# Performance work log

Hardware: AMD Instinct MI355X
Metric: run time of the kernel (lower is better)

Reference implementation:

```python
import jax, jax.numpy as jnp
import numpy as np

B, S, D = 4, 2048, 512

def setup_inputs() -> dict:
    key = jax.random.key(0)
    ks = jax.random.split(key, 7)
    # scale weights so unscaled logits stay in a sane softmax range
    w_scale = 0.05
    return {
        "x": jax.random.normal(ks[0], (B, S, D), dtype=jnp.float32),
        "W_q": jax.random.normal(ks[1], (D, D), dtype=jnp.float32) * w_scale,
        "W_k": jax.random.normal(ks[2], (D, D), dtype=jnp.float32) * w_scale,
        "W_v": jax.random.normal(ks[3], (D, D), dtype=jnp.float32) * w_scale,
        "b_q": jax.random.normal(ks[4], (D,), dtype=jnp.float32) * w_scale,
        "b_k": jax.random.normal(ks[5], (D,), dtype=jnp.float32) * w_scale,
        "b_v": jax.random.normal(ks[6], (D,), dtype=jnp.float32) * w_scale,
    }

def reference(x, W_q, W_k, W_v, b_q, b_k, b_v):
    # QKV projections: [B,S,D] @ [D,D] + [D]
    q = jnp.einsum('bsd,de->bse', x, W_q) + b_q
    k = jnp.einsum('bsd,de->bse', x, W_k) + b_k
    v = jnp.einsum('bsd,de->bse', x, W_v) + b_v
    # unscaled attention scores [B,S,S]
    scores = jnp.einsum('bqd,bkd->bqk', q, k)
    attn = jax.nn.softmax(scores, axis=-1)
    # weighted sum of values [B,S,D]
    return jnp.einsum('bqk,bkd->bqd', attn, v)
```

## Files before the change

### kernel.cpp

```cpp
#include <hip/hip_runtime.h>
#include <hip/hip_bf16.h>
#include <hip/hip_fp16.h>

#define BB 4
#define SS 2048
#define DD 512

typedef short s16x8 __attribute__((ext_vector_type(8)));
typedef short s16x4 __attribute__((ext_vector_type(4)));
typedef float f32x4 __attribute__((ext_vector_type(4)));
typedef _Float16 f16x8 __attribute__((ext_vector_type(8)));

__device__ __forceinline__ short f2h(float f) {
    const _Float16 h = (_Float16)f;
    union { _Float16 h; short s; } u; u.h = h; return u.s;
}
__device__ __forceinline__ float h2f(short s) {
    union { short s; _Float16 h; } u; u.s = s; return (float)u.h;
}
__device__ __forceinline__ f16x8 as_h(s16x8 v) {
    union { s16x8 s; f16x8 h; } u; u.s = v; return u.h;
}

__device__ __forceinline__ void gload_lds16(const void* g, void* l) {
    __builtin_amdgcn_global_load_lds(
        (const __attribute__((address_space(1))) void*)g,
        (__attribute__((address_space(3))) void*)l, 16, 0, 0);
}

__global__ __launch_bounds__(512, 2) void qkt256(
    const short* __restrict__ qf, const short* __restrict__ kf,
    short* __restrict__ outS, int nwg)
{
    __shared__ short lds[65536];

    const int tid = threadIdx.x;
    const int wave = tid >> 6, lane = tid & 63;
    const int flat = blockIdx.x + 8 * blockIdx.y + 64 * blockIdx.z;
    const int w = (flat & 7) * (nwg >> 3) + (flat >> 3);
    const int bm = ((w >> 3) & 7) * 256, bn = (w & 7) * 256;
    const long z = w >> 6;
    qf += z * (long)SS * DD; kf += z * (long)SS * DD;
    outS += z * (long)SS * SS;

    const int wm = (wave >> 2) * 128, wn = (wave & 3) * 64;
    const int lrow = lane & 15, lk16 = (lane >> 4) * 16;

    f32x4 acc[8][4] = {};

    auto base = [&](int buf, int arr) -> short* { return &lds[(buf * 2 + arr) * 8192]; };
    auto issue = [&](int buf, int arr, int k0) {
#pragma unroll
        for (int h = 0; h < 2; h++) {
            const int Lb = (h << 13) + (wave << 10) + (lane << 4);
            const int Ls = Lb ^ (((Lb >> 7) & 3) << 4);
            const int row = Ls >> 6, elem = (Ls & 63) >> 1;
            const short* s = arr ? kf : qf;
            const int rb = arr ? bn : bm;
            gload_lds16(s + (size_t)(rb + row) * DD + k0 + elem,
                        (char*)base(buf, arr) + Lb);
        }
    };
    auto rd = [&](int buf, int arr, int row) -> s16x8 {
        const int L = (row << 6) + lk16;
        const int Ls = L ^ (((L >> 7) & 3) << 4);
        return *(const s16x8*)((const char*)base(buf, arr) + Ls);
    };

#define QK_TILE(T, CUR, Bc, Bn, PREF)                                            \
  {                                                                              \
                                            \
    s16x8 aA0 = rd(CUR, 0, wm + 0 * 16 + lrow);                                  \
    s16x8 aA1 = rd(CUR, 0, wm + 1 * 16 + lrow);                                  \
    s16x8 aA2 = rd(CUR, 0, wm + 2 * 16 + lrow);                                  \
    s16x8 aA3 = rd(CUR, 0, wm + 3 * 16 + lrow);                                  \
    if (PREF) {                                                                  \
      issue((CUR) ^ 1, 1, ((T) + 1) * 32);                          \
      __builtin_amdgcn_sched_barrier(0);                                         \
      issue((CUR) ^ 1, 0, ((T) + 1) * 32);                         \
    }                                                                            \
    __builtin_amdgcn_s_barrier();                                                \
    asm volatile("s_waitcnt lgkmcnt(0)" ::: "memory");                           \
    __builtin_amdgcn_sched_barrier(0);                                           \
    __builtin_amdgcn_s_setprio(1);                                               \
    {                                                                            \
      _Pragma("unroll")                                                          \
      for (int n = 0; n < 4; n++) {                                              \
        acc[0][n] = __builtin_amdgcn_mfma_f32_16x16x32_f16(as_h(aA0), as_h(Bc[n]), acc[0][n], 0, 0, 0); \
        acc[1][n] = __builtin_amdgcn_mfma_f32_16x16x32_f16(as_h(aA1), as_h(Bc[n]), acc[1][n], 0, 0, 0); \
        acc[2][n] = __builtin_amdgcn_mfma_f32_16x16x32_f16(as_h(aA2), as_h(Bc[n]), acc[2][n], 0, 0, 0); \
        acc[3][n] = __builtin_amdgcn_mfma_f32_16x16x32_f16(as_h(aA3), as_h(Bc[n]), acc[3][n], 0, 0, 0); \
      }                                                                          \
    }                                                                            \
    __builtin_amdgcn_s_setprio(0);                                               \
    if (PREF) { asm volatile("s_waitcnt vmcnt(2)" ::: "memory");                 \
                __builtin_amdgcn_sched_barrier(0); }                             \
    __builtin_amdgcn_s_barrier();                                                \
                                            \
    aA0 = rd(CUR, 0, wm + 4 * 16 + lrow);                                        \
    aA1 = rd(CUR, 0, wm + 5 * 16 + lrow);                                        \
    aA2 = rd(CUR, 0, wm + 6 * 16 + lrow);                                        \
    aA3 = rd(CUR, 0, wm + 7 * 16 + lrow);                                        \
    if (PREF) {                                                                  \
      __builtin_amdgcn_sched_barrier(0);    \
      _Pragma("unroll")                                                          \
      for (int n = 0; n < 4; n++) {                                              \
        Bn[n] = rd((CUR) ^ 1, 1, wn + n * 16 + lrow);                            \
      }                                                                          \
    }                                                                            \
    __builtin_amdgcn_s_barrier();                                                \
    if (PREF) { asm volatile("s_waitcnt lgkmcnt(4)" ::: "memory"); }             \
    else      { asm volatile("s_waitcnt lgkmcnt(0)" ::: "memory"); }             \
    __builtin_amdgcn_sched_barrier(0);                                           \
    __builtin_amdgcn_s_setprio(1);                                               \
    {                                                                            \
      _Pragma("unroll")                                                          \
      for (int n = 0; n < 4; n++) {                                              \
        acc[4][n] = __builtin_amdgcn_mfma_f32_16x16x32_f16(as_h(aA0), as_h(Bc[n]), acc[4][n], 0, 0, 0); \
        acc[5][n] = __builtin_amdgcn_mfma_f32_16x16x32_f16(as_h(aA1), as_h(Bc[n]), acc[5][n], 0, 0, 0); \
        acc[6][n] = __builtin_amdgcn_mfma_f32_16x16x32_f16(as_h(aA2), as_h(Bc[n]), acc[6][n], 0, 0, 0); \
        acc[7][n] = __builtin_amdgcn_mfma_f32_16x16x32_f16(as_h(aA3), as_h(Bc[n]), acc[7][n], 0, 0, 0); \
      }                                                                          \
    }                                                                            \
    __builtin_amdgcn_s_setprio(0);                                               \
    if (PREF) { asm volatile("s_waitcnt vmcnt(0)" ::: "memory");                 \
                __builtin_amdgcn_sched_barrier(0); }                             \
    __builtin_amdgcn_s_barrier();                                                \
  }

    issue(0, 1, 0); issue(0, 0, 0);
    asm volatile("s_waitcnt vmcnt(0)" ::: "memory");
    __builtin_amdgcn_s_barrier();
    s16x8 bE[4], bO[4];
#pragma unroll
    for (int n = 0; n < 4; n++) bE[n] = rd(0, 1, wn + n * 16 + lrow);

    for (int t = 0; t < 14; t += 2) {
        QK_TILE(t,     0, bE, bO, 1);
        QK_TILE(t + 1, 1, bO, bE, 1);
    }
    QK_TILE(14, 0, bE, bO, 1);
    QK_TILE(15, 1, bO, bE, 0);
#undef QK_TILE

    __syncthreads();
    short* ebuf = &lds[0];
#pragma unroll
    for (int m = 0; m < 8; m++) {
#pragma unroll
        for (int n = 0; n < 4; n++) {
#pragma unroll
            for (int j = 0; j < 4; j++) {
                const int rl = wm + m * 16 + (lane >> 4) * 4 + j;
                const int cl = wn + n * 16 + lrow;
                const int pcb = (cl >> 3) ^ ((rl & 3) << 1);
                ebuf[rl * 256 + pcb * 8 + (cl & 7)] =
                    (short)__float2int_rn(acc[m][n][j] * 128.0f);
            }
        }
    }
    __syncthreads();
#pragma unroll
    for (int it = 0; it < 16; it++) {
        const int u = it * 512 + tid;
        const int R = u >> 5, cb = u & 31;
        const int pcb = cb ^ ((R & 3) << 1);
        const s16x8 val = *(const s16x8*)&ebuf[R * 256 + pcb * 8];
        *(s16x8*)&outS[(size_t)(bm + R) * SS + bn + cb * 8] = val;
    }
}

__global__ __launch_bounds__(256, 3) void proj_all(
    const short* __restrict__ xh, const short* __restrict__ xl,
    const short* __restrict__ wt,
    const float* __restrict__ bq, const float* __restrict__ bk,
    const float* __restrict__ bv,
    short* __restrict__ qfp, short* __restrict__ kfp, short* __restrict__ vt)
{
    __shared__ short As[2][128 * 64];
    __shared__ short Bs[128 * 64];

    const int tid = threadIdx.x;
    const int wave = tid >> 6, lane = tid & 63;
    const int wsel = blockIdx.x >> 2;
    const int bnl = (blockIdx.x & 3) * 128;
    const int bm = blockIdx.y * 128;
    const bool lo = (wsel < 2);
    const short* B0 = wt + (size_t)wsel * DD * DD;
    const float* bias = (wsel == 0) ? bq : (wsel == 1) ? bk : bv;

    f32x4 acc[4][4] = {};
    const int wm = (wave >> 1) * 64, wn = (wave & 1) * 64;
    const int lrow = lane & 15, lk = (lane >> 4) * 8;

    auto swz = [](int L) { return L ^ (((L >> 7) & 7) << 4); };

    for (int k0 = 0; k0 < DD; k0 += 64) {
        if (k0) __syncthreads();
#pragma unroll
        for (int r = 0; r < 4; r++) {
            const int L = tid * 16 + r * 4096;
            const int Ls = swz(L);
            const int row = Ls >> 7, col = (Ls & 127) >> 1;
            gload_lds16(xh + (size_t)(bm + row) * DD + k0 + col, (char*)&As[0][0] + L);
            gload_lds16(B0 + (size_t)(bnl + row) * DD + k0 + col, (char*)&Bs[0] + L);
            if (lo)
                gload_lds16(xl + (size_t)(bm + row) * DD + k0 + col, (char*)&As[1][0] + L);
        }
        __syncthreads();

#pragma unroll
        for (int kk = 0; kk < 64; kk += 32) {
            s16x8 ah[4], bh[4], al[4];
#pragma unroll
            for (int m = 0; m < 4; m++)
                ah[m] = *(const s16x8*)((const char*)&As[0][0] +
                        swz(((wm + m * 16 + lrow) * 64 + kk + lk) * 2));
#pragma unroll
            for (int n = 0; n < 4; n++)
                bh[n] = *(const s16x8*)((const char*)&Bs[0] +
                        swz(((wn + n * 16 + lrow) * 64 + kk + lk) * 2));
            if (lo) {
#pragma unroll
                for (int m = 0; m < 4; m++)
                    al[m] = *(const s16x8*)((const char*)&As[1][0] +
                            swz(((wm + m * 16 + lrow) * 64 + kk + lk) * 2));
            }
#pragma unroll
            for (int m = 0; m < 4; m++) {
#pragma unroll
                for (int n = 0; n < 4; n++) {
                    acc[m][n] = __builtin_amdgcn_mfma_f32_16x16x32_f16(
                        as_h(ah[m]), as_h(bh[n]), acc[m][n], 0, 0, 0);
                    if (lo)
                        acc[m][n] = __builtin_amdgcn_mfma_f32_16x16x32_f16(
                            as_h(al[m]), as_h(bh[n]), acc[m][n], 0, 0, 0);
                }
            }
        }
    }

    __syncthreads();
    short* cbuf = &As[0][0];
#pragma unroll
    for (int m = 0; m < 4; m++) {
#pragma unroll
        for (int n = 0; n < 4; n++) {
#pragma unroll
            for (int j = 0; j < 4; j++) {
                const int rl = wm + m * 16 + (lane >> 4) * 4 + j;
                const int cl = wn + n * 16 + lrow;
                const float v = acc[m][n][j] + bias[bnl + cl];
                if (wsel < 2)
                    cbuf[rl * 128 + (cl ^ ((rl & 7) << 3))] = f2h(v);
                else
                    cbuf[cl * 128 + (rl ^ ((cl & 7) << 3))] = f2h(v);
            }
        }
    }
    __syncthreads();
    if (wsel < 2) {
        short* outp = wsel ? kfp : qfp;
#pragma unroll
        for (int it = 0; it < 8; it++) {
            const int u = it * 256 + tid;
            const int r = u >> 4, c8 = (u & 15) * 8;
            const s16x8 val = *(const s16x8*)&cbuf[r * 128 + (c8 ^ ((r & 7) << 3))];
            *(s16x8*)&outp[(size_t)(bm + r) * DD + bnl + c8] = val;
        }
    } else {
        const int b = bm >> 11, s0 = bm & 2047;
#pragma unroll
        for (int it = 0; it < 8; it++) {
            const int idx = it * 256 + tid;
            const int dd = idx >> 4, c8 = (idx & 15) * 8;
            const s16x8 val = *(const s16x8*)&cbuf[dd * 128 + (c8 ^ ((dd & 7) << 3))];
            *(s16x8*)&vt[((size_t)b << 20) + ((size_t)(bnl + dd) << 11) + s0 + c8] = val;
        }
    }
}

__global__ __launch_bounds__(256, 2) void pv_gemm(
    const short* __restrict__ P, const short* __restrict__ vt,
    float* __restrict__ out)
{
    __shared__ short As[64 * 64];
    __shared__ short Bs[128 * 64];

    const int tid = threadIdx.x;
    const int wave = tid >> 6, lane = tid & 63;
    const int bm = blockIdx.y * 64, bn = blockIdx.x * 128;
    const long z = blockIdx.z;
    P += z * (long)SS * SS;
    vt += z << 20;
    out += z * (long)SS * DD;

    f32x4 acc[2][4] = {};
    const int wm = (wave >> 1) * 32, wn = (wave & 1) * 64;
    const int lrow = lane & 15, lk = (lane >> 4) * 8;

    auto swz = [](int L) { return L ^ (((L >> 7) & 7) << 4); };

    for (int k0 = 0; k0 < SS; k0 += 64) {
        if (k0) __syncthreads();
#pragma unroll
        for (int r = 0; r < 2; r++) {
            const int L = tid * 16 + r * 4096;
            const int Ls = swz(L);
            const int row = Ls >> 7, col = (Ls & 127) >> 1;
            gload_lds16(P + (size_t)(bm + row) * SS + k0 + col, (char*)&As[0] + L);
        }
#pragma unroll
        for (int r = 0; r < 4; r++) {
            const int L = tid * 16 + r * 4096;
            const int Ls = swz(L);
            const int row = Ls >> 7, col = (Ls & 127) >> 1;
            gload_lds16(vt + ((size_t)(bn + row) << 11) + k0 + col, (char*)&Bs[0] + L);
        }
        __syncthreads();

#pragma unroll
        for (int kk = 0; kk < 64; kk += 32) {
            s16x8 a[2], b[4];
#pragma unroll
            for (int m = 0; m < 2; m++)
                a[m] = *(const s16x8*)((const char*)&As[0] +
                       swz(((wm + m * 16 + lrow) * 64 + kk + lk) * 2));
#pragma unroll
            for (int n = 0; n < 4; n++)
                b[n] = *(const s16x8*)((const char*)&Bs[0] +
                       swz(((wn + n * 16 + lrow) * 64 + kk + lk) * 2));
#pragma unroll
            for (int m = 0; m < 2; m++)
#pragma unroll
                for (int n = 0; n < 4; n++)
                    acc[m][n] = __builtin_amdgcn_mfma_f32_16x16x32_f16(
                        as_h(a[m]), as_h(b[n]), acc[m][n], 0, 0, 0);
        }
    }

#pragma unroll
    for (int m = 0; m < 2; m++) {
#pragma unroll
        for (int n = 0; n < 4; n++) {
#pragma unroll
            for (int j = 0; j < 4; j++) {
                const int row = bm + wm + m * 16 + (lane >> 4) * 4 + j;
                const int col = bn + wn + n * 16 + lrow;
                out[(size_t)row * DD + col] = acc[m][n][j];
            }
        }
    }
}

__global__ __launch_bounds__(256) void cast_all(
    const float* __restrict__ x,
    const float* __restrict__ wq, const float* __restrict__ wk,
    const float* __restrict__ wv,
    short* __restrict__ xh, short* __restrict__ xl,
    short* __restrict__ wt)
{
    const int bid = blockIdx.x;
    if (bid < 4096) {
        const int i = bid * 256 + threadIdx.x;
        const float4 v = ((const float4*)x)[i];
        const float vv[4] = {v.x, v.y, v.z, v.w};
        s16x4 h, l;
#pragma unroll
        for (int j = 0; j < 4; j++) {
            const short hh = f2h(vv[j]);
            h[j] = hh;
            l[j] = f2h(vv[j] - h2f(hh));
        }
        ((s16x4*)xh)[i] = h;
        ((s16x4*)xl)[i] = l;
    } else {
        const int t = (bid - 4096) * 256 + threadIdx.x;
        const int w = t >> 18;
        const int r = t & 262143;
        const float* src = (w == 0) ? wq : ((w == 1) ? wk : wv);
        const float v = src[r];
        const int k = r >> 9, n = r & 511;
        wt[((size_t)w << 18) + ((size_t)n << 9) + k] = f2h(v);
    }
}

__global__ __launch_bounds__(256) void softmax_rows(
    const short* __restrict__ S, short* __restrict__ P)
{
    const int row = blockIdx.x;
    const long z = blockIdx.y;
    const short* s = S + z * (long)SS * SS + (long)row * SS;
    short* p = P + z * (long)SS * SS + (long)row * SS;
    const int tid = threadIdx.x;

    const s16x8 raw = ((const s16x8*)s)[tid];
    float v[8];
#pragma unroll
    for (int j = 0; j < 8; j++) v[j] = (float)(int)raw[j] * 0.0078125f;

    float m = v[0];
#pragma unroll
    for (int j = 1; j < 8; j++) m = fmaxf(m, v[j]);
#pragma unroll
    for (int off = 32; off >= 1; off >>= 1) m = fmaxf(m, __shfl_xor(m, off));
    __shared__ float redm[4], reds[4];
    if ((tid & 63) == 0) redm[tid >> 6] = m;
    __syncthreads();
    m = fmaxf(fmaxf(redm[0], redm[1]), fmaxf(redm[2], redm[3]));

    float e[8], sum = 0.f;
#pragma unroll
    for (int j = 0; j < 8; j++) { e[j] = __expf(v[j] - m); sum += e[j]; }
#pragma unroll
    for (int off = 32; off >= 1; off >>= 1) sum += __shfl_xor(sum, off);
    if ((tid & 63) == 0) reds[tid >> 6] = sum;
    __syncthreads();
    sum = reds[0] + reds[1] + reds[2] + reds[3];
    const float inv = 1.0f / sum;

    s16x8 o;
#pragma unroll
    for (int j = 0; j < 8; j++) o[j] = f2h(e[j] * inv);
    ((s16x8*)p)[tid] = o;
}

extern "C" void kernel_launch(void* const* d_in, const int* in_sizes, int n_in,
                              void* d_out, int out_size, void* d_ws, size_t ws_size,
                              hipStream_t stream)
{
    const float* x  = (const float*)d_in[0];
    const float* Wq = (const float*)d_in[1];
    const float* Wk = (const float*)d_in[2];
    const float* Wv = (const float*)d_in[3];
    const float* bq = (const float*)d_in[4];
    const float* bk = (const float*)d_in[5];
    const float* bv = (const float*)d_in[6];
    float* out = (float*)d_out;

    const size_t MK = (size_t)BB * SS * DD;
    char* ws = (char*)d_ws;
    short* xh  = (short*)ws; ws += MK * 2;
    short* xl  = (short*)ws; ws += MK * 2;
    short* wt  = (short*)ws; ws += 3ull * DD * DD * 2;
    short* qfp = (short*)ws; ws += MK * 2;
    short* kfp = (short*)ws; ws += MK * 2;
    short* vt  = (short*)ws; ws += MK * 2;
    const size_t fixed = (size_t)(ws - (char*)d_ws);

    int g = 4;
    while (g > 0 && fixed + (size_t)g * ((size_t)SS * SS * 2 + (size_t)SS * SS * 2) > ws_size)
        g >>= 1;
    if (g == 0) return;
    short* sc = (short*)ws;
    short* P  = (short*)(ws + (size_t)g * SS * SS * 2);

    cast_all<<<dim3(7168), 256, 0, stream>>>(x, Wq, Wk, Wv, xh, xl, wt);
    proj_all<<<dim3(12, 64), 256, 0, stream>>>(xh, xl, wt, bq, bk, bv,
                                               qfp, kfp, vt);

    for (int b0 = 0; b0 < BB; b0 += g) {
        const int gg = (b0 + g <= BB) ? g : (BB - b0);
        qkt256<<<dim3(8, 8, gg), 512, 0, stream>>>(
            qfp + (size_t)b0 * SS * DD, kfp + (size_t)b0 * SS * DD, sc, 64 * gg);
        softmax_rows<<<dim3(SS, gg), 256, 0, stream>>>(sc, P);
        pv_gemm<<<dim3(4, 32, gg), 256, 0, stream>>>(
            P, vt + ((size_t)b0 << 20), out + (size_t)b0 * SS * DD);
    }
}
```

Baseline: 118.1 us.

## Double-buffer projection and PV GEMMs with async LDS prefetch; simplify QK tile pipeline

Rewrites the QKV projection and P·V GEMMs to use double-buffered LDS with global_load_lds prefetch of the next k-tile issued before the MFMA block, so loads overlap compute, replacing the single-buffer load/sync/compute loops. The QK^T kernel's two-phase split tile with interleaved B-fragment prefetch is collapsed into one phase per tile that reads all fragments, then issues the prefetch. pv_gemm occupancy hint rises to 3 blocks per CU despite doubled LDS. Risks include higher register pressure from holding all fragments, and the simpler QK pipeline may hide less latency than the old split version.

```diff
diff --git a/kernel.cpp b/kernel.cpp
--- a/kernel.cpp
+++ b/kernel.cpp
@@ -27,6 +27,10 @@
         (const __attribute__((address_space(1))) void*)g,
         (__attribute__((address_space(3))) void*)l, 16, 0, 0);
 }
+
+#define SB0 __builtin_amdgcn_sched_barrier(0)
+#define LGKM0 asm volatile("s_waitcnt lgkmcnt(0)" ::: "memory")
+#define VM0   asm volatile("s_waitcnt vmcnt(0)" ::: "memory")
 
 __global__ __launch_bounds__(512, 2) void qkt256(
     const short* __restrict__ qf, const short* __restrict__ kf,
@@ -52,7 +56,7 @@
     auto issue = [&](int buf, int arr, int k0) {
 #pragma unroll
         for (int h = 0; h < 2; h++) {
-            const int Lb = (h << 13) + (wave << 10) + (lane << 4);
+            const int Lb = (h << 13) + (tid << 4);
             const int Ls = Lb ^ (((Lb >> 7) & 3) << 4);
             const int row = Ls >> 6, elem = (Ls & 63) >> 1;
             const short* s = arr ? kf : qf;
@@ -67,80 +71,37 @@
         return *(const s16x8*)((const char*)base(buf, arr) + Ls);
     };
 
-#define QK_TILE(T, CUR, Bc, Bn, PREF)                                            \
+#define QK_TILE(T, CUR, PREF)                                                    \
   {                                                                              \
-                                            \
-    s16x8 aA0 = rd(CUR, 0, wm + 0 * 16 + lrow);                                  \
-    s16x8 aA1 = rd(CUR, 0, wm + 1 * 16 + lrow);                                  \
-    s16x8 aA2 = rd(CUR, 0, wm + 2 * 16 + lrow);                                  \
-    s16x8 aA3 = rd(CUR, 0, wm + 3 * 16 + lrow);                                  \
-    if (PREF) {                                                                  \
-      issue((CUR) ^ 1, 1, ((T) + 1) * 32);                          \
-      __builtin_amdgcn_sched_barrier(0);                                         \
-      issue((CUR) ^ 1, 0, ((T) + 1) * 32);                         \
-    }                                                                            \
-    __builtin_amdgcn_s_barrier();                                                \
-    asm volatile("s_waitcnt lgkmcnt(0)" ::: "memory");                           \
-    __builtin_amdgcn_sched_barrier(0);                                           \
+    s16x8 a[8], b[4];                                                            \
+    _Pragma("unroll")                                                            \
+    for (int m = 0; m < 8; m++) a[m] = rd(CUR, 0, wm + m * 16 + lrow);           \
+    _Pragma("unroll")                                                            \
+    for (int n = 0; n < 4; n++) b[n] = rd(CUR, 1, wn + n * 16 + lrow);           \
+    if (PREF) { issue((CUR) ^ 1, 1, ((T) + 1) * 32); SB0;                        \
+                issue((CUR) ^ 1, 0, ((T) + 1) * 32); }                           \
+    LGKM0; SB0;                                                                  \
     __builtin_amdgcn_s_setprio(1);                                               \
-    {                                                                            \
-      _Pragma("unroll")                                                          \
-      for (int n = 0; n < 4; n++) {                                              \
-        acc[0][n] = __builtin_amdgcn_mfma_f32_16x16x32_f16(as_h(aA0), as_h(Bc[n]), acc[0][n], 0, 0, 0); \
-        acc[1][n] = __builtin_amdgcn_mfma_f32_16x16x32_f16(as_h(aA1), as_h(Bc[n]), acc[1][n], 0, 0, 0); \
-        acc[2][n] = __builtin_amdgcn_mfma_f32_16x16x32_f16(as_h(aA2), as_h(Bc[n]), acc[2][n], 0, 0, 0); \
-        acc[3][n] = __builtin_amdgcn_mfma_f32_16x16x32_f16(as_h(aA3), as_h(Bc[n]), acc[3][n], 0, 0, 0); \
-      }                                                                          \
+    _Pragma("unroll")                                                            \
+    for (int m = 0; m < 8; m++) {                                                \
+      _Pragma("unroll")                                                          \
+      for (int n = 0; n < 4; n++)                                                \
+        acc[m][n] = __builtin_amdgcn_mfma_f32_16x16x32_f16(                      \
+            as_h(a[m]), as_h(b[n]), acc[m][n], 0, 0, 0);                         \
     }                                                                            \
     __builtin_amdgcn_s_setprio(0);                                               \
-    if (PREF) { asm volatile("s_waitcnt vmcnt(2)" ::: "memory");                 \
-                __builtin_amdgcn_sched_barrier(0); }                             \
-    __builtin_amdgcn_s_barrier();                                                \
-                                            \
-    aA0 = rd(CUR, 0, wm + 4 * 16 + lrow);                                        \
-    aA1 = rd(CUR, 0, wm + 5 * 16 + lrow);                                        \
-    aA2 = rd(CUR, 0, wm + 6 * 16 + lrow);                                        \
-    aA3 = rd(CUR, 0, wm + 7 * 16 + lrow);                                        \
-    if (PREF) {                                                                  \
-      __builtin_amdgcn_sched_barrier(0);    \
-      _Pragma("unroll")                                                          \
-      for (int n = 0; n < 4; n++) {                                              \
-        Bn[n] = rd((CUR) ^ 1, 1, wn + n * 16 + lrow);                            \
-      }                                                                          \
-    }                                                                            \
-    __builtin_amdgcn_s_barrier();                                                \
-    if (PREF) { asm volatile("s_waitcnt lgkmcnt(4)" ::: "memory"); }             \
-    else      { asm volatile("s_waitcnt lgkmcnt(0)" ::: "memory"); }             \
-    __builtin_amdgcn_sched_barrier(0);                                           \
-    __builtin_amdgcn_s_setprio(1);                                               \
-    {                                                                            \
-      _Pragma("unroll")                                                          \
-      for (int n = 0; n < 4; n++) {                                              \
-        acc[4][n] = __builtin_amdgcn_mfma_f32_16x16x32_f16(as_h(aA0), as_h(Bc[n]), acc[4][n], 0, 0, 0); \
-        acc[5][n] = __builtin_amdgcn_mfma_f32_16x16x32_f16(as_h(aA1), as_h(Bc[n]), acc[5][n], 0, 0, 0); \
-        acc[6][n] = __builtin_amdgcn_mfma_f32_16x16x32_f16(as_h(aA2), as_h(Bc[n]), acc[6][n], 0, 0, 0); \
-        acc[7][n] = __builtin_amdgcn_mfma_f32_16x16x32_f16(as_h(aA3), as_h(Bc[n]), acc[7][n], 0, 0, 0); \
-      }                                                                          \
-    }                                                                            \
-    __builtin_amdgcn_s_setprio(0);                                               \
-    if (PREF) { asm volatile("s_waitcnt vmcnt(0)" ::: "memory");                 \
-                __builtin_amdgcn_sched_barrier(0); }                             \
+    if (PREF) { VM0; SB0; }                                                      \
     __builtin_amdgcn_s_barrier();                                                \
   }
 
     issue(0, 1, 0); issue(0, 0, 0);
-    asm volatile("s_waitcnt vmcnt(0)" ::: "memory");
+    VM0;
     __builtin_amdgcn_s_barrier();
-    s16x8 bE[4], bO[4];
-#pragma unroll
-    for (int n = 0; n < 4; n++) bE[n] = rd(0, 1, wn + n * 16 + lrow);
-
-    for (int t = 0; t < 14; t += 2) {
-        QK_TILE(t,     0, bE, bO, 1);
-        QK_TILE(t + 1, 1, bO, bE, 1);
-    }
-    QK_TILE(14, 0, bE, bO, 1);
-    QK_TILE(15, 1, bO, bE, 0);
+
+    for (int t = 0; t < 16; t += 2) {
+        QK_TILE(t,     0, 1);
+        QK_TILE(t + 1, 1, (t + 1) < 15);
+    }
 #undef QK_TILE
 
     __syncthreads();
@@ -177,8 +138,7 @@
     const float* __restrict__ bv,
     short* __restrict__ qfp, short* __restrict__ kfp, short* __restrict__ vt)
 {
-    __shared__ short As[2][128 * 64];
-    __shared__ short Bs[128 * 64];
+    __shared__ short lds[24576];
 
     const int tid = threadIdx.x;
     const int wave = tid >> 6, lane = tid & 63;
@@ -191,57 +151,74 @@
 
     f32x4 acc[4][4] = {};
     const int wm = (wave >> 1) * 64, wn = (wave & 1) * 64;
-    const int lrow = lane & 15, lk = (lane >> 4) * 8;
-
-    auto swz = [](int L) { return L ^ (((L >> 7) & 7) << 4); };
-
-    for (int k0 = 0; k0 < DD; k0 += 64) {
-        if (k0) __syncthreads();
-#pragma unroll
-        for (int r = 0; r < 4; r++) {
-            const int L = tid * 16 + r * 4096;
-            const int Ls = swz(L);
-            const int row = Ls >> 7, col = (Ls & 127) >> 1;
-            gload_lds16(xh + (size_t)(bm + row) * DD + k0 + col, (char*)&As[0][0] + L);
-            gload_lds16(B0 + (size_t)(bnl + row) * DD + k0 + col, (char*)&Bs[0] + L);
-            if (lo)
-                gload_lds16(xl + (size_t)(bm + row) * DD + k0 + col, (char*)&As[1][0] + L);
-        }
-        __syncthreads();
-
-#pragma unroll
-        for (int kk = 0; kk < 64; kk += 32) {
-            s16x8 ah[4], bh[4], al[4];
-#pragma unroll
-            for (int m = 0; m < 4; m++)
-                ah[m] = *(const s16x8*)((const char*)&As[0][0] +
-                        swz(((wm + m * 16 + lrow) * 64 + kk + lk) * 2));
-#pragma unroll
-            for (int n = 0; n < 4; n++)
-                bh[n] = *(const s16x8*)((const char*)&Bs[0] +
-                        swz(((wn + n * 16 + lrow) * 64 + kk + lk) * 2));
-            if (lo) {
-#pragma unroll
-                for (int m = 0; m < 4; m++)
-                    al[m] = *(const s16x8*)((const char*)&As[1][0] +
-                            swz(((wm + m * 16 + lrow) * 64 + kk + lk) * 2));
-            }
-#pragma unroll
-            for (int m = 0; m < 4; m++) {
-#pragma unroll
-                for (int n = 0; n < 4; n++) {
-                    acc[m][n] = __builtin_amdgcn_mfma_f32_16x16x32_f16(
-                        as_h(ah[m]), as_h(bh[n]), acc[m][n], 0, 0, 0);
-                    if (lo)
-                        acc[m][n] = __builtin_amdgcn_mfma_f32_16x16x32_f16(
-                            as_h(al[m]), as_h(bh[n]), acc[m][n], 0, 0, 0);
-                }
-            }
-        }
-    }
-
-    __syncthreads();
-    short* cbuf = &As[0][0];
+    const int lrow = lane & 15, lk16 = (lane >> 4) * 16;
+
+    auto base = [&](int buf, int arr) -> short* { return &lds[(buf * 3 + arr) * 4096]; };
+    auto issue = [&](int buf, int arr, int k0) {
+#pragma unroll
+        for (int h = 0; h < 2; h++) {
+            const int Lb = (h << 12) + (tid << 4);
+            const int Ls = Lb ^ (((Lb >> 7) & 3) << 4);
+            const int row = Ls >> 6, elem = (Ls & 63) >> 1;
+            const short* s = (arr == 0) ? xh : (arr == 1) ? xl : B0;
+            const int rb = (arr < 2) ? bm : bnl;
+            gload_lds16(s + (size_t)(rb + row) * DD + k0 + elem,
+                        (char*)base(buf, arr) + Lb);
+        }
+    };
+    auto rd = [&](int buf, int arr, int row) -> s16x8 {
+        const int L = (row << 6) + lk16;
+        const int Ls = L ^ (((L >> 7) & 3) << 4);
+        return *(const s16x8*)((const char*)base(buf, arr) + Ls);
+    };
+
+#define PJ_TILE(T, CUR, PREF)                                                    \
+  {                                                                              \
+    s16x8 ah[4], al[4], b[4];                                                    \
+    _Pragma("unroll")                                                            \
+    for (int m = 0; m < 4; m++) ah[m] = rd(CUR, 0, wm + m * 16 + lrow);          \
+    if (lo) {                                                                    \
+      _Pragma("unroll")                                                          \
+      for (int m = 0; m < 4; m++) al[m] = rd(CUR, 1, wm + m * 16 + lrow);        \
+    }                                                                            \
+    _Pragma("unroll")                                                            \
+    for (int n = 0; n < 4; n++) b[n] = rd(CUR, 2, wn + n * 16 + lrow);           \
+    if (PREF) {                                                                  \
+      issue((CUR) ^ 1, 2, ((T) + 1) * 32); SB0;                                  \
+      issue((CUR) ^ 1, 0, ((T) + 1) * 32);                                       \
+      if (lo) issue((CUR) ^ 1, 1, ((T) + 1) * 32);                               \
+    }                                                                            \
+    LGKM0; SB0;                                                                  \
+    __builtin_amdgcn_s_setprio(1);                                               \
+    _Pragma("unroll")                                                            \
+    for (int m = 0; m < 4; m++) {                                                \
+      _Pragma("unroll")                                                          \
+      for (int n = 0; n < 4; n++) {                                              \
+        acc[m][n] = __builtin_amdgcn_mfma_f32_16x16x32_f16(                      \
+            as_h(ah[m]), as_h(b[n]), acc[m][n], 0, 0, 0);                        \
+        if (lo)                                                                  \
+          acc[m][n] = __builtin_amdgcn_mfma_f32_16x16x32_f16(                    \
+              as_h(al[m]), as_h(b[n]), acc[m][n], 0, 0, 0);                      \
+      }                                                                          \
+    }                                                                            \
+    __builtin_amdgcn_s_setprio(0);                                               \
+    if (PREF) { VM0; SB0; }                                                      \
+    __builtin_amdgcn_s_barrier();                                                \
+  }
+
+    issue(0, 2, 0); issue(0, 0, 0);
+    if (lo) issue(0, 1, 0);
+    VM0;
+    __builtin_amdgcn_s_barrier();
+
+    for (int t = 0; t < 16; t += 2) {
+        PJ_TILE(t,     0, 1);
+        PJ_TILE(t + 1, 1, (t + 1) < 15);
+    }
+#undef PJ_TILE
+
+    __syncthreads();
+    short* cbuf = &lds[0];
 #pragma unroll
     for (int m = 0; m < 4; m++) {
 #pragma unroll
@@ -280,12 +257,12 @@
     }
 }
 
-__global__ __launch_bounds__(256, 2) void pv_gemm(
+__global__ __launch_bounds__(256, 3) void pv_gemm(
     const short* __restrict__ P, const short* __restrict__ vt,
     float* __restrict__ out)
 {
-    __shared__ short As[64 * 64];
-    __shared__ short Bs[128 * 64];
+    __shared__ short As[2][64 * 64];
+    __shared__ short Bs[2][128 * 64];
 
     const int tid = threadIdx.x;
     const int wave = tid >> 6, lane = tid & 63;
@@ -300,44 +277,67 @@
     const int lrow = lane & 15, lk = (lane >> 4) * 8;
 
     auto swz = [](int L) { return L ^ (((L >> 7) & 7) << 4); };
-
-    for (int k0 = 0; k0 < SS; k0 += 64) {
-        if (k0) __syncthreads();
-#pragma unroll
-        for (int r = 0; r < 2; r++) {
-            const int L = tid * 16 + r * 4096;
+    auto issueA = [&](int buf, int k0) {
+#pragma unroll
+        for (int h = 0; h < 2; h++) {
+            const int L = (h << 12) + (tid << 4);
             const int Ls = swz(L);
             const int row = Ls >> 7, col = (Ls & 127) >> 1;
-            gload_lds16(P + (size_t)(bm + row) * SS + k0 + col, (char*)&As[0] + L);
-        }
-#pragma unroll
-        for (int r = 0; r < 4; r++) {
-            const int L = tid * 16 + r * 4096;
+            gload_lds16(P + (size_t)(bm + row) * SS + k0 + col, (char*)&As[buf][0] + L);
+        }
+    };
+    auto issueB = [&](int buf, int k0) {
+#pragma unroll
+        for (int h = 0; h < 4; h++) {
+            const int L = (h << 12) + (tid << 4);
             const int Ls = swz(L);
             const int row = Ls >> 7, col = (Ls & 127) >> 1;
-            gload_lds16(vt + ((size_t)(bn + row) << 11) + k0 + col, (char*)&Bs[0] + L);
-        }
-        __syncthreads();
-
-#pragma unroll
-        for (int kk = 0; kk < 64; kk += 32) {
-            s16x8 a[2], b[4];
-#pragma unroll
-            for (int m = 0; m < 2; m++)
-                a[m] = *(const s16x8*)((const char*)&As[0] +
-                       swz(((wm + m * 16 + lrow) * 64 + kk + lk) * 2));
-#pragma unroll
-            for (int n = 0; n < 4; n++)
-                b[n] = *(const s16x8*)((const char*)&Bs[0] +
-                       swz(((wn + n * 16 + lrow) * 64 + kk + lk) * 2));
-#pragma unroll
-            for (int m = 0; m < 2; m++)
-#pragma unroll
-                for (int n = 0; n < 4; n++)
-                    acc[m][n] = __builtin_amdgcn_mfma_f32_16x16x32_f16(
-                        as_h(a[m]), as_h(b[n]), acc[m][n], 0, 0, 0);
-        }
-    }
+            gload_lds16(vt + ((size_t)(bn + row) << 11) + k0 + col, (char*)&Bs[buf][0] + L);
+        }
+    };
+
+#define PV_TILE(T, CUR, PREF)                                                    \
+  {                                                                              \
+    s16x8 a[2][2], b[2][4];                                                      \
+    _Pragma("unroll")                                                            \
+    for (int kx = 0; kx < 2; kx++) {                                             \
+      _Pragma("unroll")                                                          \
+      for (int m = 0; m < 2; m++)                                                \
+        a[kx][m] = *(const s16x8*)((const char*)&As[CUR][0] +                    \
+                   swz(((wm + m * 16 + lrow) * 64 + kx * 32 + lk) * 2));         \
+      _Pragma("unroll")                                                          \
+      for (int n = 0; n < 4; n++)                                                \
+        b[kx][n] = *(const s16x8*)((const char*)&Bs[CUR][0] +                    \
+                   swz(((wn + n * 16 + lrow) * 64 + kx * 32 + lk) * 2));         \
+    }                                                                            \
+    if (PREF) { issueB((CUR) ^ 1, ((T) + 1) * 64); SB0;                          \
+                issueA((CUR) ^ 1, ((T) + 1) * 64); }                             \
+    LGKM0; SB0;                                                                  \
+    __builtin_amdgcn_s_setprio(1);                                               \
+    _Pragma("unroll")                                                            \
+    for (int kx = 0; kx < 2; kx++) {                                             \
+      _Pragma("unroll")                                                          \
+      for (int m = 0; m < 2; m++) {                                              \
+        _Pragma("unroll")                                                        \
+        for (int n = 0; n < 4; n++)                                              \
+          acc[m][n] = __builtin_amdgcn_mfma_f32_16x16x32_f16(                    \
+              as_h(a[kx][m]), as_h(b[kx][n]), acc[m][n], 0, 0, 0);               \
+      }                                                                          \
+    }                                                                            \
+    __builtin_amdgcn_s_setprio(0);                                               \
+    if (PREF) { VM0; SB0; }                                                      \
+    __builtin_amdgcn_s_barrier();                                                \
+  }
+
+    issueB(0, 0); issueA(0, 0);
+    VM0;
+    __builtin_amdgcn_s_barrier();
+
+    for (int t = 0; t < 32; t += 2) {
+        PV_TILE(t,     0, 1);
+        PV_TILE(t + 1, 1, (t + 1) < 31);
+    }
+#undef PV_TILE
 
 #pragma unroll
     for (int m = 0; m < 2; m++) {
```

After: 116.5 us. No clear change (-1.3%).
